# Performance work log

Hardware: AMD Instinct MI355X
Metric: run time of the kernel (lower is better)

## Reference

```python
import jax, jax.numpy as jnp
import numpy as np

TAG = 64
START = 0
END = 1
NEG = -10000.0


def setup_inputs() -> dict:
    key = jax.random.key(0)
    kf, kw, kl = jax.random.split(key, 3)
    B, T, K = 1024, 512, TAG
    feats = jax.random.normal(kf, (B, T, K), dtype=jnp.float32)
    w = jax.random.uniform(kw, (K, K), minval=-1.0 / K, maxval=1.0 / K, dtype=jnp.float32)
    # default adjacency: forbid transitions into start (row START) and out of end (col END)
    adj = jnp.zeros((K, K), jnp.float32).at[START, :].set(1.0).at[:, END].set(1.0)
    weights = w + NEG * adj
    lens = jax.random.randint(kl, (B,), 1, T + 1)  # 1..T inclusive
    return {"feats": feats, "weights": weights, "lens": lens}


def reference(feats, weights, lens):
    # feats: [B, T, K], weights: [K, K] with weights[next, prev], lens: [B]
    B, T, K = feats.shape
    init = jnp.full((B, K), NEG, feats.dtype).at[:, START].set(0.0)
    mask_tb = (jnp.arange(T)[None, :] < lens[:, None]).T  # [T, B]
    ident = jnp.arange(K, dtype=jnp.int32)

    def step(fv, inp):
        feat, m = inp  # feat: [B, K], m: [B]
        scores = fv[:, None, :] + weights[None, :, :]  # [B, next, prev]
        new_fv = jnp.max(scores, axis=-1) + feat       # emission added after max
        bptr = jnp.argmax(scores, axis=-1).astype(jnp.int32)
        fv2 = jnp.where(m[:, None], new_fv, fv)
        bptr2 = jnp.where(m[:, None], bptr, ident[None, :])  # identity keeps backtrace valid past len
        return fv2, bptr2

    fv, bptrs = jax.lax.scan(step, init, (jnp.swapaxes(feats, 0, 1), mask_tb))
    terminal = fv + weights[END][None, :]              # transition to end tag
    best_last = jnp.argmax(terminal, axis=-1)
    path_score = jnp.take_along_axis(terminal, best_last[:, None], axis=1)[:, 0]

    def back(tag, bp):  # tag: [B], bp: [B, K]
        prev = jnp.take_along_axis(bp, tag[:, None], axis=1)[:, 0]
        return prev, tag  # emit tag chosen at this timestep

    _, path = jax.lax.scan(back, best_last.astype(jnp.int32), bptrs, reverse=True)
    best_paths = jnp.swapaxes(path, 0, 1)  # [B, T]; positions >= lens[b] are padding
    return path_score, best_paths
```

## Files before the change

kernel.cpp:

```cpp
#include <hip/hip_runtime.h>

#define TAGS 64
#define MAXT 512
#define NEG  -10000.0f
#define CH   8

__global__ __launch_bounds__(64, 1) void crf_viterbi(
    const float* __restrict__ feats,
    const float* __restrict__ weights,
    const int*   __restrict__ lens,
    float*       __restrict__ out,
    int B, int T)
{
    const int b    = blockIdx.x;
    const int lane = threadIdx.x;
    const int len  = lens[b];

    __shared__ unsigned char  bptr[MAXT * TAGS];
    __shared__ unsigned short path[MAXT];

    float wf[TAGS];
    #pragma unroll
    for (int i = 0; i < 16; ++i) {
        const float4 q = *reinterpret_cast<const float4*>(weights + lane * TAGS + i * 4);
        wf[4*i+0] = q.x; wf[4*i+1] = q.y; wf[4*i+2] = q.z; wf[4*i+3] = q.w;
    }
    const float wEnd = weights[1 * TAGS + lane];

    const float* fb  = feats + (size_t)b * T * TAGS;
    const int    cap = len * TAGS;

    float nf = (lane == 0) ? 0.0f : NEG;

#define F3(a, b, c) fmaxf(fmaxf((a), (b)), (c))
#define M3(a, b, c) min(min((a), (b)), (c))

    auto step = [&](float feat, int t) {
        float c[64];
        #pragma unroll
        for (int p = 0; p < 64; ++p) {
            const float fvp = __uint_as_float(
                __builtin_amdgcn_readlane(__float_as_uint(nf), p));
            c[p] = fvp + wf[p];
        }

        float v1[22];
        #pragma unroll
        for (int k = 0; k < 21; ++k) v1[k] = F3(c[3*k], c[3*k+1], c[3*k+2]);
        v1[21] = c[63];
        float v2[8];
        #pragma unroll
        for (int k = 0; k < 7; ++k) v2[k] = F3(v1[3*k], v1[3*k+1], v1[3*k+2]);
        v2[7] = v1[21];
        const float v30 = F3(v2[0], v2[1], v2[2]);
        const float v31 = F3(v2[3], v2[4], v2[5]);
        const float v32 = fmaxf(v2[6], v2[7]);
        const float m   = F3(v30, v31, v32);

        nf = m + feat;

        unsigned e[64];
        #pragma unroll
        for (int p = 0; p < 64; ++p) e[p] = (c[p] == m) ? (unsigned)p : 64u;
        unsigned u1[22];
        #pragma unroll
        for (int k = 0; k < 21; ++k) u1[k] = M3(e[3*k], e[3*k+1], e[3*k+2]);
        u1[21] = e[63];
        unsigned u2[8];
        #pragma unroll
        for (int k = 0; k < 7; ++k) u2[k] = M3(u1[3*k], u1[3*k+1], u1[3*k+2]);
        u2[7] = u1[21];
        const unsigned u30 = M3(u2[0], u2[1], u2[2]);
        const unsigned u31 = M3(u2[3], u2[4], u2[5]);
        const unsigned u32 = min(u2[6], u2[7]);
        const unsigned idx = M3(u30, u31, u32);

        bptr[t * TAGS + lane] = (unsigned char)idx;
    };

    float fcur[CH], fnx[CH];
    #pragma unroll
    for (int i = 0; i < CH; ++i) {
        int o = i * TAGS + lane; if (o >= cap) o = lane;
        fcur[i] = fb[o];
    }
    #pragma unroll
    for (int i = 0; i < CH; ++i) {
        int o = (CH + i) * TAGS + lane; if (o >= cap) o = lane;
        fnx[i] = fb[o];
    }

    const int nfull = len / CH;
    for (int ch = 0; ch < nfull; ++ch) {
        #pragma unroll
        for (int i = 0; i < CH; ++i) step(fcur[i], ch * CH + i);
        #pragma unroll
        for (int i = 0; i < CH; ++i) fcur[i] = fnx[i];
        #pragma unroll
        for (int i = 0; i < CH; ++i) {
            int o = (ch + 2) * CH * TAGS + i * TAGS + lane; if (o >= cap) o = lane;
            fnx[i] = fb[o];
        }
    }
    const int rem = len - nfull * CH;
    #pragma unroll
    for (int i = 0; i < CH; ++i)
        if (i < rem) step(fcur[i], nfull * CH + i);

    float tv = nf + wEnd;
    int   ti = lane;
    #pragma unroll
    for (int off = 32; off >= 1; off >>= 1) {
        const float ov = __shfl_xor(tv, off);
        const int   oi = __shfl_xor(ti, off);
        if (ov > tv || (ov == tv && oi < ti)) { tv = ov; ti = oi; }
    }
    if (lane == 0) out[b] = tv;
    const int bestlast = ti;

    for (int t = lane; t < T; t += 64)
        if (t >= len - 1) path[t] = (unsigned short)bestlast;
    __builtin_amdgcn_wave_barrier();

    if (lane == 0) {
        int tag = bestlast;
        for (int t = len - 1; t >= 1; --t) {
            tag = bptr[t * TAGS + tag];
            path[t - 1] = (unsigned short)tag;
        }
    }
    __builtin_amdgcn_wave_barrier();

    float* pout = out + B + (size_t)b * T;
    for (int t = lane; t < T; t += 64)
        pout[t] = (float)path[t];
}

extern "C" void kernel_launch(void* const* d_in, const int* in_sizes, int n_in,
                              void* d_out, int out_size, void* d_ws, size_t ws_size,
                              hipStream_t stream) {
    const float* feats   = (const float*)d_in[0];
    const float* weights = (const float*)d_in[1];
    const int*   lens    = (const int*)d_in[2];
    float*       out     = (float*)d_out;

    const int B = in_sizes[2];
    const int T = in_sizes[0] / (B * TAGS);

    crf_viterbi<<<dim3(B), dim3(64), 0, stream>>>(feats, weights, lens, out, B, T);
}
```

Baseline: 441.5 us.

## Split Viterbi into a max-recurrence producer wave and argmax consumer waves

Each block now runs three waves. Wave 0 carries only the serial forward max recurrence and writes each step's forward vector into a double-buffered shared array. Two consumer waves redo the 64-way max and the argmax for the previous chunk, writing the backpointers. This takes the argmax index reduction off the serial dependency chain. In exchange it adds a __syncthreads per chunk of 8 steps, redundant max work in the consumers, and higher register and occupancy pressure per block.

```diff
diff --git a/kernel.cpp b/kernel.cpp
--- a/kernel.cpp
+++ b/kernel.cpp
@@ -4,8 +4,9 @@
 #define MAXT 512
 #define NEG  -10000.0f
 #define CH   8
+#define NCONS 2
 
-__global__ __launch_bounds__(64, 1) void crf_viterbi(
+__global__ __launch_bounds__(192, 3) void crf_viterbi(
     const float* __restrict__ feats,
     const float* __restrict__ weights,
     const int*   __restrict__ lens,
@@ -13,11 +14,17 @@
     int B, int T)
 {
     const int b    = blockIdx.x;
-    const int lane = threadIdx.x;
+    const int tid  = threadIdx.x;
+    const int wv   = tid >> 6;
+    const int lane = tid & 63;
     const int len  = lens[b];
 
     __shared__ unsigned char  bptr[MAXT * TAGS];
     __shared__ unsigned short path[MAXT];
+    __shared__ float fvbuf[2][CH][TAGS];
+
+#define F3(a, b, c) fmaxf(fmaxf((a), (b)), (c))
+#define M3(a, b, c) min(min((a), (b)), (c))
 
     float wf[TAGS];
     #pragma unroll
@@ -29,21 +36,11 @@
 
     const float* fb  = feats + (size_t)b * T * TAGS;
     const int    cap = len * TAGS;
+    const int    nch = (len + CH - 1) / CH;
 
     float nf = (lane == 0) ? 0.0f : NEG;
 
-#define F3(a, b, c) fmaxf(fmaxf((a), (b)), (c))
-#define M3(a, b, c) min(min((a), (b)), (c))
-
-    auto step = [&](float feat, int t) {
-        float c[64];
-        #pragma unroll
-        for (int p = 0; p < 64; ++p) {
-            const float fvp = __uint_as_float(
-                __builtin_amdgcn_readlane(__float_as_uint(nf), p));
-            c[p] = fvp + wf[p];
-        }
-
+    auto maxtree = [&](const float* c) -> float {
         float v1[22];
         #pragma unroll
         for (int k = 0; k < 21; ++k) v1[k] = F3(c[3*k], c[3*k+1], c[3*k+2]);
@@ -55,10 +52,9 @@
         const float v30 = F3(v2[0], v2[1], v2[2]);
         const float v31 = F3(v2[3], v2[4], v2[5]);
         const float v32 = fmaxf(v2[6], v2[7]);
-        const float m   = F3(v30, v31, v32);
-
-        nf = m + feat;
-
+        return F3(v30, v31, v32);
+    };
+    auto argscan = [&](const float* c, float m) -> unsigned {
         unsigned e[64];
         #pragma unroll
         for (int p = 0; p < 64; ++p) e[p] = (c[p] == m) ? (unsigned)p : 64u;
@@ -73,39 +69,71 @@
         const unsigned u30 = M3(u2[0], u2[1], u2[2]);
         const unsigned u31 = M3(u2[3], u2[4], u2[5]);
         const unsigned u32 = min(u2[6], u2[7]);
-        const unsigned idx = M3(u30, u31, u32);
-
-        bptr[t * TAGS + lane] = (unsigned char)idx;
+        return M3(u30, u31, u32);
     };
 
     float fcur[CH], fnx[CH];
-    #pragma unroll
-    for (int i = 0; i < CH; ++i) {
-        int o = i * TAGS + lane; if (o >= cap) o = lane;
-        fcur[i] = fb[o];
-    }
-    #pragma unroll
-    for (int i = 0; i < CH; ++i) {
-        int o = (CH + i) * TAGS + lane; if (o >= cap) o = lane;
-        fnx[i] = fb[o];
-    }
-
-    const int nfull = len / CH;
-    for (int ch = 0; ch < nfull; ++ch) {
-        #pragma unroll
-        for (int i = 0; i < CH; ++i) step(fcur[i], ch * CH + i);
-        #pragma unroll
-        for (int i = 0; i < CH; ++i) fcur[i] = fnx[i];
+    if (wv == 0) {
         #pragma unroll
         for (int i = 0; i < CH; ++i) {
-            int o = (ch + 2) * CH * TAGS + i * TAGS + lane; if (o >= cap) o = lane;
+            int o = i * TAGS + lane; if (o >= cap) o = lane;
+            fcur[i] = fb[o];
+        }
+        #pragma unroll
+        for (int i = 0; i < CH; ++i) {
+            int o = (CH + i) * TAGS + lane; if (o >= cap) o = lane;
             fnx[i] = fb[o];
         }
     }
-    const int rem = len - nfull * CH;
-    #pragma unroll
-    for (int i = 0; i < CH; ++i)
-        if (i < rem) step(fcur[i], nfull * CH + i);
+
+    for (int c = 0; c <= nch; ++c) {
+        if (wv == 0 && c < nch) {
+            const int n = min(CH, len - c * CH);
+            fvbuf[c & 1][0][lane] = nf;
+            #pragma unroll
+            for (int i = 0; i < CH; ++i) {
+                if (i < n) {
+                    float cv[64];
+                    #pragma unroll
+                    for (int p = 0; p < 64; ++p) {
+                        const float fvp = __uint_as_float(
+                            __builtin_amdgcn_readlane(__float_as_uint(nf), p));
+                        cv[p] = fvp + wf[p];
+                    }
+                    nf = maxtree(cv) + fcur[i];
+                    if (i + 1 < CH) fvbuf[c & 1][i + 1][lane] = nf;
+                }
+            }
+            #pragma unroll
+            for (int i = 0; i < CH; ++i) fcur[i] = fnx[i];
+            #pragma unroll
+            for (int i = 0; i < CH; ++i) {
+                int o = (c + 2) * CH * TAGS + i * TAGS + lane; if (o >= cap) o = lane;
+                fnx[i] = fb[o];
+            }
+        }
+        if (wv > 0 && c > 0) {
+            const int cc = c - 1;
+            const int n  = min(CH, len - cc * CH);
+            for (int i = wv - 1; i < n; i += NCONS) {
+                float cv[64];
+                #pragma unroll
+                for (int g = 0; g < 16; ++g) {
+                    const float4 q = *reinterpret_cast<const float4*>(&fvbuf[cc & 1][i][4 * g]);
+                    cv[4*g+0] = q.x + wf[4*g+0];
+                    cv[4*g+1] = q.y + wf[4*g+1];
+                    cv[4*g+2] = q.z + wf[4*g+2];
+                    cv[4*g+3] = q.w + wf[4*g+3];
+                }
+                const float    m   = maxtree(cv);
+                const unsigned idx = argscan(cv, m);
+                bptr[(cc * CH + i) * TAGS + lane] = (unsigned char)idx;
+            }
+        }
+        __syncthreads();
+    }
+
+    if (wv != 0) return;
 
     float tv = nf + wEnd;
     int   ti = lane;
@@ -147,5 +175,5 @@
     const int B = in_sizes[2];
     const int T = in_sizes[0] / (B * TAGS);
 
-    crf_viterbi<<<dim3(B), dim3(64), 0, stream>>>(feats, weights, lens, out, B, T);
+    crf_viterbi<<<dim3(B), dim3(192), 0, stream>>>(feats, weights, lens, out, B, T);
 }
```

Result: slower. 531.8 us (+20.4%).

## Split Viterbi max over two waves with LDS-shared forward vector

Applied to the files above, without the earlier changes.

Each block now runs two waves. Each lane handles one next-tag and half of the 64 previous tags, the two halves are combined with a cross-half shuffle, and the forward vector is exchanged through double-buffered shared memory. The 64 readlane broadcasts are replaced with vector LDS loads. The argmax now packs m - c and the index into one integer key and takes a min. The aim is to halve the serial per-step work and get more parallelism per block, at the cost of a __syncthreads on every timestep.

```diff
diff --git a/kernel.cpp b/kernel.cpp
--- a/kernel.cpp
+++ b/kernel.cpp
@@ -5,7 +5,7 @@
 #define NEG  -10000.0f
 #define CH   8
 
-__global__ __launch_bounds__(64, 1) void crf_viterbi(
+__global__ __launch_bounds__(128, 1) void crf_viterbi(
     const float* __restrict__ feats,
     const float* __restrict__ weights,
     const int*   __restrict__ lens,
@@ -13,92 +13,109 @@
     int B, int T)
 {
     const int b    = blockIdx.x;
-    const int lane = threadIdx.x;
+    const int tid  = threadIdx.x;
+    const int wid  = tid >> 6;
+    const int lane = tid & 63;
+    const int n    = wid * 32 + (lane & 31);
+    const int h    = lane >> 5;
     const int len  = lens[b];
 
+    __shared__ float fvbuf[2][TAGS];
     __shared__ unsigned char  bptr[MAXT * TAGS];
     __shared__ unsigned short path[MAXT];
 
-    float wf[TAGS];
+#define F3(a, b, c) fmaxf(fmaxf((a), (b)), (c))
+#define M3(a, b, c) min(min((a), (b)), (c))
+
+    float4 w4[8];
     #pragma unroll
-    for (int i = 0; i < 16; ++i) {
-        const float4 q = *reinterpret_cast<const float4*>(weights + lane * TAGS + i * 4);
-        wf[4*i+0] = q.x; wf[4*i+1] = q.y; wf[4*i+2] = q.z; wf[4*i+3] = q.w;
-    }
+    for (int g = 0; g < 8; ++g)
+        w4[g] = *reinterpret_cast<const float4*>(weights + n * TAGS + h * 32 + 4 * g);
     const float wEnd = weights[1 * TAGS + lane];
 
     const float* fb  = feats + (size_t)b * T * TAGS;
     const int    cap = len * TAGS;
 
-    float nf = (lane == 0) ? 0.0f : NEG;
-
-#define F3(a, b, c) fmaxf(fmaxf((a), (b)), (c))
-#define M3(a, b, c) min(min((a), (b)), (c))
-
-    auto step = [&](float feat, int t) {
-        float c[64];
-        #pragma unroll
-        for (int p = 0; p < 64; ++p) {
-            const float fvp = __uint_as_float(
-                __builtin_amdgcn_readlane(__float_as_uint(nf), p));
-            c[p] = fvp + wf[p];
-        }
-
-        float v1[22];
-        #pragma unroll
-        for (int k = 0; k < 21; ++k) v1[k] = F3(c[3*k], c[3*k+1], c[3*k+2]);
-        v1[21] = c[63];
-        float v2[8];
-        #pragma unroll
-        for (int k = 0; k < 7; ++k) v2[k] = F3(v1[3*k], v1[3*k+1], v1[3*k+2]);
-        v2[7] = v1[21];
-        const float v30 = F3(v2[0], v2[1], v2[2]);
-        const float v31 = F3(v2[3], v2[4], v2[5]);
-        const float v32 = fmaxf(v2[6], v2[7]);
-        const float m   = F3(v30, v31, v32);
-
-        nf = m + feat;
-
-        unsigned e[64];
-        #pragma unroll
-        for (int p = 0; p < 64; ++p) e[p] = (c[p] == m) ? (unsigned)p : 64u;
-        unsigned u1[22];
-        #pragma unroll
-        for (int k = 0; k < 21; ++k) u1[k] = M3(e[3*k], e[3*k+1], e[3*k+2]);
-        u1[21] = e[63];
-        unsigned u2[8];
-        #pragma unroll
-        for (int k = 0; k < 7; ++k) u2[k] = M3(u1[3*k], u1[3*k+1], u1[3*k+2]);
-        u2[7] = u1[21];
-        const unsigned u30 = M3(u2[0], u2[1], u2[2]);
-        const unsigned u31 = M3(u2[3], u2[4], u2[5]);
-        const unsigned u32 = min(u2[6], u2[7]);
-        const unsigned idx = M3(u30, u31, u32);
-
-        bptr[t * TAGS + lane] = (unsigned char)idx;
-    };
-
     float fcur[CH], fnx[CH];
     #pragma unroll
     for (int i = 0; i < CH; ++i) {
-        int o = i * TAGS + lane; if (o >= cap) o = lane;
+        int o = i * TAGS + n; if (o >= cap) o = n;
         fcur[i] = fb[o];
     }
     #pragma unroll
     for (int i = 0; i < CH; ++i) {
-        int o = (CH + i) * TAGS + lane; if (o >= cap) o = lane;
+        int o = (CH + i) * TAGS + n; if (o >= cap) o = n;
         fnx[i] = fb[o];
     }
 
+    if (tid < 64) fvbuf[0][lane] = (lane == 0) ? 0.0f : NEG;
+    __syncthreads();
+
+    int cur = 0;
+    float nf = NEG;
+
+    auto step = [&](float feat, int t) {
+        const float* fvh = &fvbuf[cur][h * 32];
+        float4 c4[8];
+        #pragma unroll
+        for (int g = 0; g < 8; ++g) {
+            const float4 fq = *reinterpret_cast<const float4*>(fvh + 4 * g);
+            c4[g].x = fq.x + w4[g].x;
+            c4[g].y = fq.y + w4[g].y;
+            c4[g].z = fq.z + w4[g].z;
+            c4[g].w = fq.w + w4[g].w;
+        }
+        const float* cc = reinterpret_cast<const float*>(c4);
+
+        float v1[11];
+        #pragma unroll
+        for (int k = 0; k < 10; ++k) v1[k] = F3(cc[3*k], cc[3*k+1], cc[3*k+2]);
+        v1[10] = fmaxf(cc[30], cc[31]);
+        const float v20 = F3(v1[0], v1[1], v1[2]);
+        const float v21 = F3(v1[3], v1[4], v1[5]);
+        const float v22 = F3(v1[6], v1[7], v1[8]);
+        const float v23 = fmaxf(v1[9], v1[10]);
+        const float mh  = fmaxf(F3(v20, v21, v22), v23);
+
+        const float mo = __shfl_xor(mh, 32);
+        const float m  = fmaxf(mh, mo);
+
+        nf = m + feat;
+        if (lane < 32) fvbuf[cur ^ 1][n] = nf;
+
+        unsigned q[8];
+        #pragma unroll
+        for (int g = 0; g < 8; ++g) {
+            const int p = h * 32 + 4 * g;
+            const unsigned k0 = (__float_as_uint(m - c4[g].x) & 0xFFFFFFC0u) | (unsigned)(p + 0);
+            const unsigned k1 = (__float_as_uint(m - c4[g].y) & 0xFFFFFFC0u) | (unsigned)(p + 1);
+            const unsigned k2 = (__float_as_uint(m - c4[g].z) & 0xFFFFFFC0u) | (unsigned)(p + 2);
+            const unsigned k3 = (__float_as_uint(m - c4[g].w) & 0xFFFFFFC0u) | (unsigned)(p + 3);
+            q[g] = min(M3(k0, k1, k2), k3);
+        }
+        const unsigned u0 = M3(q[0], q[1], q[2]);
+        const unsigned u1 = M3(q[3], q[4], q[5]);
+        const unsigned u2 = min(q[6], q[7]);
+        const unsigned uh = M3(u0, u1, u2);
+        const unsigned uo = __shfl_xor(uh, 32);
+        const unsigned idx = min(uh, uo);
+
+        if (lane < 32) bptr[t * TAGS + n] = (unsigned char)idx;
+
+        __syncthreads();
+        cur ^= 1;
+    };
+
     const int nfull = len / CH;
-    for (int ch = 0; ch < nfull; ++ch) {
+    for (int c = 0; c < nfull; ++c) {
         #pragma unroll
-        for (int i = 0; i < CH; ++i) step(fcur[i], ch * CH + i);
+        for (int i = 0; i < CH; ++i) step(fcur[i], c * CH + i);
         #pragma unroll
         for (int i = 0; i < CH; ++i) fcur[i] = fnx[i];
         #pragma unroll
         for (int i = 0; i < CH; ++i) {
-            int o = (ch + 2) * CH * TAGS + i * TAGS + lane; if (o >= cap) o = lane;
+            int o = (c + 2) * CH * TAGS + i * TAGS + n;
+            if (o >= cap) o = n;
             fnx[i] = fb[o];
         }
     }
@@ -107,7 +124,11 @@
     for (int i = 0; i < CH; ++i)
         if (i < rem) step(fcur[i], nfull * CH + i);
 
-    float tv = nf + wEnd;
+    if (wid != 0) return;
+
+    const float fvl = fvbuf[cur][lane];
+
+    float tv = fvl + wEnd;
     int   ti = lane;
     #pragma unroll
     for (int off = 32; off >= 1; off >>= 1) {
@@ -147,5 +168,5 @@
     const int B = in_sizes[2];
     const int T = in_sizes[0] / (B * TAGS);
 
-    crf_viterbi<<<dim3(B), dim3(64), 0, stream>>>(feats, weights, lens, out, B, T);
+    crf_viterbi<<<dim3(B), dim3(128), 0, stream>>>(feats, weights, lens, out, B, T);
 }
```

New measurement: 449.2 us. Within noise of the previous version (+1.7%).
